# Kernel optimization log

Hardware: AMD Instinct MI355X
Metric: run time of the kernel (lower is better)

Reference implementation:

```python
import jax, jax.numpy as jnp
import numpy as np


def _lstm_layer(x_seq, w_ih, w_hh, b_ih, b_hh):
    # x_seq: [T, in], PyTorch gate order i, f, g, o
    H = w_hh.shape[1]
    h0 = jnp.zeros((H,), x_seq.dtype)

    def step(carry, x_t):
        h, c = carry
        gates = x_t @ w_ih.T + h @ w_hh.T + b_ih + b_hh  # [4H]
        i, f, g, o = jnp.split(gates, 4)
        i = jax.nn.sigmoid(i)
        f = jax.nn.sigmoid(f)
        g = jnp.tanh(g)
        o = jax.nn.sigmoid(o)
        c = f * c + i * g
        h = o * jnp.tanh(c)
        return (h, c), h

    _, hs = jax.lax.scan(step, (h0, h0), x_seq)
    return hs  # [T, H]


def setup_inputs() -> dict:
    key = jax.random.key(0)
    ks = jax.random.split(key, 12)
    B, T, n, H = 8, 128, 32, 128
    s = 1.0 / np.sqrt(H)

    def u(k, shape):
        return jax.random.uniform(k, shape, jnp.float32, -s, s)

    return {
        "x": jax.random.normal(ks[0], (B, T, n, n), jnp.float32),
        "w_ih0": u(ks[1], (4 * H, 1)),
        "w_hh0": u(ks[2], (4 * H, H)),
        "b_ih0": u(ks[3], (4 * H,)),
        "b_hh0": u(ks[4], (4 * H,)),
        "w_ih1": u(ks[5], (4 * H, H)),
        "w_hh1": u(ks[6], (4 * H, H)),
        "b_ih1": u(ks[7], (4 * H,)),
        "b_hh1": u(ks[8], (4 * H,)),
        "w_out": u(ks[9], (1, H)),
        "b_out": u(ks[10], (1,)),
    }


def reference(x, w_ih0, w_hh0, b_ih0, b_hh0, w_ih1, w_hh1, b_ih1, b_hh1, w_out, b_out):
    # x: [B, T, n, n]
    def rnn_forward(xi):  # xi: [T, n, n] -> out [T, 1]
        u = jnp.trace(xi, axis1=-2, axis2=-1)[:, None]  # [T, 1]
        h1 = _lstm_layer(u, w_ih0, w_hh0, b_ih0, b_hh0)
        h2 = _lstm_layer(h1, w_ih1, w_hh1, b_ih1, b_hh1)
        return h2 @ w_out.T + b_out  # [T, 1]

    jac = jax.vmap(jax.jacrev(rnn_forward))(x)  # [B, T, 1, T, n, n]
    d = jnp.diagonal(jac, axis1=1, axis2=3)      # [B, 1, n, n, T]
    # mirror torch: [:, 0] then transpose(2,3).transpose(1,2) -> [B, T, n, n]
    return jnp.transpose(d[:, 0], (0, 3, 1, 2))
```

## Files before the change

### kernel.cpp

```cpp
#include <hip/hip_runtime.h>
#include <math.h>

#define H    128
#define TT   128
#define CH   8
#define NCH  (TT / CH)

#define OFF_H1V   0
#define OFF_PARTS 262144
#define OFF_CNT   1441792

typedef __attribute__((ext_vector_type(2))) float f2;

__device__ __forceinline__ float sigf(float x)       { return 1.0f / (1.0f + __expf(-x)); }
__device__ __forceinline__ float tanhf_fast(float x) { return 1.0f - 2.0f / (1.0f + __expf(2.0f * x)); }

__device__ __forceinline__ float quad_sum(float v) {
    int t = __builtin_amdgcn_update_dpp(0, __float_as_int(v), 0xB1, 0xF, 0xF, true);
    v += __int_as_float(t);
    t = __builtin_amdgcn_update_dpp(0, __float_as_int(v), 0x4E, 0xF, 0xF, true);
    v += __int_as_float(t);
    return v;
}

__device__ __forceinline__ void wait_ge(int* ptr, int val) {
    while (__hip_atomic_load(ptr, __ATOMIC_RELAXED, __HIP_MEMORY_SCOPE_AGENT) < val)
        __builtin_amdgcn_s_sleep(1);
    (void)__hip_atomic_load(ptr, __ATOMIC_ACQUIRE, __HIP_MEMORY_SCOPE_AGENT);
}

#define BARRIER_LGKM() do { \
    asm volatile("s_waitcnt lgkmcnt(0)" ::: "memory"); \
    __builtin_amdgcn_s_barrier(); \
    asm volatile("" ::: "memory"); \
} while (0)

#define BARRIER_ALL() do { \
    asm volatile("s_waitcnt vmcnt(0) lgkmcnt(0)" ::: "memory"); \
    __builtin_amdgcn_s_barrier(); \
    asm volatile("" ::: "memory"); \
} while (0)

#define DECLW4(nm, src) \
    float4 _t_##nm = (src); \
    f2 nm##_a = {_t_##nm.x, _t_##nm.y}; \
    f2 nm##_b = {_t_##nm.z, _t_##nm.w}; \
    asm volatile("" : "+v"(nm##_a), "+v"(nm##_b));

#define LOADW_ALL(W) \
    const float4* wpa_ = (const float4*)((W) + (size_t)(rg)       * H + p * 32); \
    const float4* wpb_ = (const float4*)((W) + (size_t)(rg + 128) * H + p * 32); \
    const float4* wpc_ = (const float4*)((W) + (size_t)(rg + 256) * H + p * 32); \
    const float4* wpd_ = (const float4*)((W) + (size_t)(rg + 384) * H + p * 32); \
    DECLW4(wa0, wpa_[0]) DECLW4(wa1, wpa_[1]) DECLW4(wa2, wpa_[2]) DECLW4(wa3, wpa_[3]) \
    DECLW4(wa4, wpa_[4]) DECLW4(wa5, wpa_[5]) DECLW4(wa6, wpa_[6]) DECLW4(wa7, wpa_[7]) \
    DECLW4(wb0, wpb_[0]) DECLW4(wb1, wpb_[1]) DECLW4(wb2, wpb_[2]) DECLW4(wb3, wpb_[3]) \
    DECLW4(wb4, wpb_[4]) DECLW4(wb5, wpb_[5]) DECLW4(wb6, wpb_[6]) DECLW4(wb7, wpb_[7]) \
    DECLW4(wc0, wpc_[0]) DECLW4(wc1, wpc_[1]) DECLW4(wc2, wpc_[2]) DECLW4(wc3, wpc_[3]) \
    DECLW4(wc4, wpc_[4]) DECLW4(wc5, wpc_[5]) DECLW4(wc6, wpc_[6]) DECLW4(wc7, wpc_[7]) \
    DECLW4(wd0, wpd_[0]) DECLW4(wd1, wpd_[1]) DECLW4(wd2, wpd_[2]) DECLW4(wd3, wpd_[3]) \
    DECLW4(wd4, wpd_[4]) DECLW4(wd5, wpd_[5]) DECLW4(wd6, wpd_[6]) DECLW4(wd7, wpd_[7])

#define PKFMA(acc, w, h) \
    asm("v_pk_fma_f32 %0, %1, %2, %0" : "+v"(acc) : "v"(w), "v"(h));

#define FMA1(nm, hA, hB, acc) PKFMA(acc, nm##_a, hA) PKFMA(acc, nm##_b, hB)

#define DOTJ(j) { \
    f2 hA_ = {hv##j.x, hv##j.y}; f2 hB_ = {hv##j.z, hv##j.w}; \
    FMA1(wa##j, hA_, hB_, q0) FMA1(wb##j, hA_, hB_, q1) \
    FMA1(wc##j, hA_, hB_, q2) FMA1(wd##j, hA_, hB_, q3) }

#define DOT_BODY(HBASE) \
    const float4* _hp4 = (const float4*)(HBASE); \
    float4 hv0=_hp4[0],hv1=_hp4[1],hv2=_hp4[2],hv3=_hp4[3], \
           hv4=_hp4[4],hv5=_hp4[5],hv6=_hp4[6],hv7=_hp4[7]; \
    f2 q0={0.f,0.f},q1={0.f,0.f},q2={0.f,0.f},q3={0.f,0.f}; \
    DOTJ(0) DOTJ(1) DOTJ(2) DOTJ(3) DOTJ(4) DOTJ(5) DOTJ(6) DOTJ(7) \
    float a0=q0.x+q0.y, a1=q1.x+q1.y, a2=q2.x+q2.y, a3=q3.x+q3.y; \
    a0 = quad_sum(a0); a1 = quad_sum(a1); a2 = quad_sum(a2); a3 = quad_sum(a3);

__global__ __launch_bounds__(512)
__attribute__((amdgpu_waves_per_eu(1, 2)))
void pipe_kernel(const float* __restrict__ x,
                 const float* __restrict__ w_ih0,
                 const float* __restrict__ w_hh0,
                 const float* __restrict__ b_ih0,
                 const float* __restrict__ b_hh0,
                 const float* __restrict__ w_ih1,
                 const float* __restrict__ w_hh1,
                 const float* __restrict__ b_ih1,
                 const float* __restrict__ b_hh1,
                 const float* __restrict__ w_out,
                 float* __restrict__ ws,
                 float* __restrict__ outp) {
    const int role = blockIdx.x >> 3;
    const int b    = blockIdx.x & 7;
    const int r    = threadIdx.x;
    const int rg   = r >> 2, p = r & 3;
    const int wsl  = rg >> 5, wpos = rg & 31;

    int* cntA  = (int*)ws + OFF_CNT       + b * 32;
    int* cntB1 = (int*)ws + OFF_CNT + 256 + b * 32;
    int* cntB2 = (int*)ws + OFF_CNT + 512 + b * 32;
    float* h1v = ws + OFF_H1V + (size_t)b * TT * 256;

    __shared__ float hbuf[2][144];
    __shared__ float u_s[TT];
    __shared__ float scr[512];
    __shared__ float hb[CH * 144];
    __shared__ float gbuf[CH][128];

    if (role == 0) {
        LOADW_ALL(w_hh0)
        const float b0 = b_ih0[rg]       + b_hh0[rg];
        const float b1 = b_ih0[rg + 128] + b_hh0[rg + 128];
        const float b2 = b_ih0[rg + 256] + b_hh0[rg + 256];
        const float b3 = b_ih0[rg + 384] + b_hh0[rg + 384];
        const float wi0 = w_ih0[rg], wi1 = w_ih0[rg + 128];
        const float wi2 = w_ih0[rg + 256], wi3 = w_ih0[rg + 384];
        {
            const float* xb = x + (size_t)(b * TT + (r & 127)) * 1024;
            const int pq = r >> 7;
            float u = 0.f;
#pragma unroll
            for (int i = 0; i < 8; i++) u += xb[(pq * 8 + i) * 33];
            scr[r] = u;
        }
        if (r < 144) hbuf[0][r] = 0.f;
        __syncthreads();
        if (r < TT) u_s[r] = scr[r] + scr[r + 128] + scr[r + 256] + scr[r + 384];
        __syncthreads();

        float c1 = 0.f;
        float hn_prev = 0.f, vn_prev = 0.f;
        for (int t = 0; t < TT; t++) {
            if (t > 0) {
                if (p == 0) h1v[(t - 1) * 256 + rg] = hn_prev;
                if (p == 1) h1v[(t - 1) * 256 + 128 + rg] = vn_prev;
            }
            const float u = u_s[t];
            const float* hc = hbuf[t & 1];
            float* hx = hbuf[(t & 1) ^ 1];
            DOT_BODY(hc + p * 36)
            float z0 = a0 + fmaf(wi0, u, b0);
            float z1 = a1 + fmaf(wi1, u, b1);
            float z2 = a2 + fmaf(wi2, u, b2);
            float z3 = a3 + fmaf(wi3, u, b3);
            float gi = sigf(z0), gf = sigf(z1), gg = tanhf_fast(z2), go = sigf(z3);
            float di = gi * (1.f - gi) * wi0, df = gf * (1.f - gf) * wi1;
            float dg = (1.f - gg * gg) * wi2, dd = go * (1.f - go) * wi3;
            float dc = df * c1 + di * gg + gi * dg;
            c1 = gf * c1 + gi * gg;
            float th = tanhf_fast(c1);
            float hn = go * th;
            float vn = dd * th + go * (1.f - th * th) * dc;
            if (p == wsl) hx[p * 36 + wpos] = hn;
            hn_prev = hn; vn_prev = vn;
            if ((t & (CH - 1)) == 0 && t > 0) {
                BARRIER_ALL();
                if (r == 0)
                    __hip_atomic_store(cntA, t, __ATOMIC_RELEASE, __HIP_MEMORY_SCOPE_AGENT);
            } else {
                BARRIER_LGKM();
            }
        }
        if (p == 0) h1v[(TT - 1) * 256 + rg] = hn_prev;
        if (p == 1) h1v[(TT - 1) * 256 + 128 + rg] = vn_prev;
        BARRIER_ALL();
        if (r == 0)
            __hip_atomic_store(cntA, TT, __ATOMIC_RELEASE, __HIP_MEMORY_SCOPE_AGENT);
    } else if (role == 1 || role == 2) {
        LOADW_ALL(w_ih1)
        int* myCnt = (role == 2) ? cntB2 : cntB1;
        const float* hsrc = h1v + ((role == 2) ? 128 : 0);
        float* pbase = ws + OFF_PARTS + (size_t)b * TT * 1024 + ((role == 2) ? 512 : 0);
        for (int c = 0; c < NCH; c++) {
            if (r == 0) wait_ge(cntA, (c + 1) * CH);
            __syncthreads();
            if (r < 256) {
                int tl = r >> 5, k4 = r & 31, s = k4 >> 3, j = k4 & 7;
                float4 v = *(const float4*)(hsrc + (size_t)(c * CH + tl) * 256 + k4 * 4);
                *(float4*)&hb[(tl * 4 + s) * 36 + j * 4] = v;
            }
            __syncthreads();
#pragma unroll
            for (int tl = 0; tl < CH; tl++) {
                DOT_BODY(hb + (tl * 4 + p) * 36)
                float sel = (p == 0) ? a0 : (p == 1) ? a1 : (p == 2) ? a2 : a3;
                pbase[(size_t)(c * CH + tl) * 1024 + r] = sel;
            }
            BARRIER_ALL();
            if (r == 0)
                __hip_atomic_store(myCnt, (c + 1) * CH, __ATOMIC_RELEASE, __HIP_MEMORY_SCOPE_AGENT);
        }
    } else {
        LOADW_ALL(w_hh1)
        const float b0 = b_ih1[rg]       + b_hh1[rg];
        const float b1 = b_ih1[rg + 128] + b_hh1[rg + 128];
        const float b2 = b_ih1[rg + 256] + b_hh1[rg + 256];
        const float b3 = b_ih1[rg + 384] + b_hh1[rg + 384];
        const float wo = w_out[rg];
        if (r < 144) hbuf[0][r] = 0.f;
        __syncthreads();
        const float* parts = ws + OFF_PARTS + (size_t)b * TT * 1024;
        float c2 = 0.f;
        for (int c = 0; c < NCH; c++) {
            if (r == 0) { wait_ge(cntB1, (c + 1) * CH); wait_ge(cntB2, (c + 1) * CH); }
            __syncthreads();
            float4 zf[CH], af[CH];
#pragma unroll
            for (int tl = 0; tl < CH; tl++) {
                zf[tl] = *(const float4*)(parts + (size_t)(c * CH + tl) * 1024 + rg * 4);
                af[tl] = *(const float4*)(parts + (size_t)(c * CH + tl) * 1024 + 512 + rg * 4);
            }
#pragma unroll
            for (int tl = 0; tl < CH; tl++) {
                const int t = c * CH + tl;
                const float* hc = hbuf[t & 1];
                float* hx = hbuf[(t & 1) ^ 1];
                DOT_BODY(hc + p * 36)
                float z0 = a0 + b0 + zf[tl].x;
                float z1 = a1 + b1 + zf[tl].y;
                float z2 = a2 + b2 + zf[tl].z;
                float z3 = a3 + b3 + zf[tl].w;
                float gi = sigf(z0), gf = sigf(z1), gg = tanhf_fast(z2), go = sigf(z3);
                float di = gi * (1.f - gi) * af[tl].x, df = gf * (1.f - gf) * af[tl].y;
                float dg = (1.f - gg * gg) * af[tl].z, dd = go * (1.f - go) * af[tl].w;
                float dc = df * c2 + di * gg + gi * dg;
                c2 = gf * c2 + gi * gg;
                float th = tanhf_fast(c2);
                if (p == wsl) hx[p * 36 + wpos] = go * th;
                float dh2 = dd * th + go * (1.f - th * th) * dc;
                if (p == 0) gbuf[tl][rg] = wo * dh2;
                BARRIER_LGKM();
            }
            {
                const int w = r >> 6, l = r & 63;
                float v = gbuf[w][l] + gbuf[w][l + 64];
                v = quad_sum(v);
                v += __shfl_xor(v, 4, 64);
                v += __shfl_xor(v, 8, 64);
                v += __shfl_xor(v, 16, 64);
                v += __shfl_xor(v, 32, 64);
                if (l == 0) scr[w] = v;
                BARRIER_LGKM();
                if (r < 256) {
                    const int tl = r >> 5, d = r & 31;
                    outp[(size_t)(b * TT + c * CH + tl) * 1024 + d * 33] = scr[tl];
                }
            }
        }
    }
}

extern "C" void kernel_launch(void* const* d_in, const int* in_sizes, int n_in,
                              void* d_out, int out_size, void* d_ws, size_t ws_size,
                              hipStream_t stream) {
    const float* x     = (const float*)d_in[0];
    const float* w_ih0 = (const float*)d_in[1];
    const float* w_hh0 = (const float*)d_in[2];
    const float* b_ih0 = (const float*)d_in[3];
    const float* b_hh0 = (const float*)d_in[4];
    const float* w_ih1 = (const float*)d_in[5];
    const float* w_hh1 = (const float*)d_in[6];
    const float* b_ih1 = (const float*)d_in[7];
    const float* b_hh1 = (const float*)d_in[8];
    const float* w_out = (const float*)d_in[9];

    float* ws = (float*)d_ws;

    hipMemsetAsync(d_out, 0, (size_t)out_size, stream);

    pipe_kernel<<<dim3(32), dim3(512), 0, stream>>>(x, w_ih0, w_hh0, b_ih0, b_hh0,
                                                    w_ih1, w_hh1, b_ih1, b_hh1, w_out,
                                                    ws, (float*)d_out);
}
```

Before: 235.3 us.

## Defer layer-2 output reduction into next chunk and use hardware reciprocal

Double-buffers gbuf so the per-chunk output reduction and store run at the start of the next chunk, sharing the barrier with the wait for producer counters. This removes one barrier per chunk. The two counter waits now run in parallel on different threads instead of one after the other, which shortens the serial spin. The sigmoid and tanh helpers also switch from IEEE division to the approximate hardware reciprocal, which cuts per-step latency but lowers precision slightly.

```diff
diff --git a/kernel.cpp b/kernel.cpp
--- a/kernel.cpp
+++ b/kernel.cpp
@@ -12,8 +12,9 @@
 
 typedef __attribute__((ext_vector_type(2))) float f2;
 
-__device__ __forceinline__ float sigf(float x)       { return 1.0f / (1.0f + __expf(-x)); }
-__device__ __forceinline__ float tanhf_fast(float x) { return 1.0f - 2.0f / (1.0f + __expf(2.0f * x)); }
+__device__ __forceinline__ float rcpf(float x) { return __builtin_amdgcn_rcpf(x); }
+__device__ __forceinline__ float sigf(float x)       { return rcpf(1.0f + __expf(-x)); }
+__device__ __forceinline__ float tanhf_fast(float x) { return 1.0f - 2.0f * rcpf(1.0f + __expf(2.0f * x)); }
 
 __device__ __forceinline__ float quad_sum(float v) {
     int t = __builtin_amdgcn_update_dpp(0, __float_as_int(v), 0xB1, 0xF, 0xF, true);
@@ -109,7 +110,7 @@
     __shared__ float u_s[TT];
     __shared__ float scr[512];
     __shared__ float hb[CH * 144];
-    __shared__ float gbuf[CH][128];
+    __shared__ float gbuf[2][CH][128];
 
     if (role == 0) {
         LOADW_ALL(w_hh0)
@@ -206,8 +207,23 @@
         const float* parts = ws + OFF_PARTS + (size_t)b * TT * 1024;
         float c2 = 0.f;
         for (int c = 0; c < NCH; c++) {
-            if (r == 0) { wait_ge(cntB1, (c + 1) * CH); wait_ge(cntB2, (c + 1) * CH); }
+            if (r == 448) wait_ge(cntB1, (c + 1) * CH);
+            if (r == 449) wait_ge(cntB2, (c + 1) * CH);
+            if (c > 0) {
+                const int w = r >> 6, l = r & 63;
+                float v = gbuf[(c - 1) & 1][w][l] + gbuf[(c - 1) & 1][w][l + 64];
+                v = quad_sum(v);
+                v += __shfl_xor(v, 4, 64);
+                v += __shfl_xor(v, 8, 64);
+                v += __shfl_xor(v, 16, 64);
+                v += __shfl_xor(v, 32, 64);
+                if (l == 0) scr[w] = v;
+            }
             __syncthreads();
+            if (c > 0 && r < 256) {
+                const int tl = r >> 5, d = r & 31;
+                outp[(size_t)(b * TT + (c - 1) * CH + tl) * 1024 + d * 33] = scr[tl];
+            }
             float4 zf[CH], af[CH];
 #pragma unroll
             for (int tl = 0; tl < CH; tl++) {
@@ -232,23 +248,23 @@
                 float th = tanhf_fast(c2);
                 if (p == wsl) hx[p * 36 + wpos] = go * th;
                 float dh2 = dd * th + go * (1.f - th * th) * dc;
-                if (p == 0) gbuf[tl][rg] = wo * dh2;
+                if (p == 0) gbuf[c & 1][tl][rg] = wo * dh2;
                 BARRIER_LGKM();
             }
-            {
-                const int w = r >> 6, l = r & 63;
-                float v = gbuf[w][l] + gbuf[w][l + 64];
-                v = quad_sum(v);
-                v += __shfl_xor(v, 4, 64);
-                v += __shfl_xor(v, 8, 64);
-                v += __shfl_xor(v, 16, 64);
-                v += __shfl_xor(v, 32, 64);
-                if (l == 0) scr[w] = v;
-                BARRIER_LGKM();
-                if (r < 256) {
-                    const int tl = r >> 5, d = r & 31;
-                    outp[(size_t)(b * TT + c * CH + tl) * 1024 + d * 33] = scr[tl];
-                }
+        }
+        {
+            const int w = r >> 6, l = r & 63;
+            float v = gbuf[(NCH - 1) & 1][w][l] + gbuf[(NCH - 1) & 1][w][l + 64];
+            v = quad_sum(v);
+            v += __shfl_xor(v, 4, 64);
+            v += __shfl_xor(v, 8, 64);
+            v += __shfl_xor(v, 16, 64);
+            v += __shfl_xor(v, 32, 64);
+            if (l == 0) scr[w] = v;
+            BARRIER_LGKM();
+            if (r < 256) {
+                const int tl = r >> 5, d = r & 31;
+                outp[(size_t)(b * TT + (NCH - 1) * CH + tl) * 1024 + d * 33] = scr[tl];
             }
         }
     }
```

New measurement: 224.8 us. 4.5% less time.

## Shrink pipeline tail chunks and defer output reduction into next round

Applied to the files above, without the earlier changes.

The last chunk of the layer-0 → input-projection → layer-1 pipeline is split into two half-size chunks, so the downstream stages can start earlier and the serial tail latency shrinks. The layer-1 stage now double-buffers its gradient buffer and folds the previous chunk's cross-row reduction and output scatter into the next round's barrier. This removes one dedicated barrier per chunk from the serial recurrence. The counter waits are spread across two threads. Sigmoid and tanh also switch from a full division to the hardware reciprocal, which lowers ALU latency at a small cost in precision.

```diff
diff --git a/kernel.cpp b/kernel.cpp
--- a/kernel.cpp
+++ b/kernel.cpp
@@ -4,7 +4,6 @@
 #define H    128
 #define TT   128
 #define CH   8
-#define NCH  (TT / CH)
 
 #define OFF_H1V   0
 #define OFF_PARTS 262144
@@ -12,8 +11,9 @@
 
 typedef __attribute__((ext_vector_type(2))) float f2;
 
-__device__ __forceinline__ float sigf(float x)       { return 1.0f / (1.0f + __expf(-x)); }
-__device__ __forceinline__ float tanhf_fast(float x) { return 1.0f - 2.0f / (1.0f + __expf(2.0f * x)); }
+__device__ __forceinline__ float rcpf(float x) { return __builtin_amdgcn_rcpf(x); }
+__device__ __forceinline__ float sigf(float x)       { return rcpf(1.0f + __expf(-x)); }
+__device__ __forceinline__ float tanhf_fast(float x) { return 1.0f - 2.0f * rcpf(1.0f + __expf(2.0f * x)); }
 
 __device__ __forceinline__ float quad_sum(float v) {
     int t = __builtin_amdgcn_update_dpp(0, __float_as_int(v), 0xB1, 0xF, 0xF, true);
@@ -79,6 +79,75 @@
     DOTJ(0) DOTJ(1) DOTJ(2) DOTJ(3) DOTJ(4) DOTJ(5) DOTJ(6) DOTJ(7) \
     float a0=q0.x+q0.y, a1=q1.x+q1.y, a2=q2.x+q2.y, a3=q3.x+q3.y; \
     a0 = quad_sum(a0); a1 = quad_sum(a1); a2 = quad_sum(a2); a3 = quad_sum(a3);
+
+#define B_ROUND(cstart, clen) { \
+    if (r == 0) wait_ge(cntA, (cstart) + (clen)); \
+    __syncthreads(); \
+    if (r < (clen) * 32) { \
+        int tl = r >> 5, k4 = r & 31, s = k4 >> 3, j = k4 & 7; \
+        float4 v = *(const float4*)(hsrc + (size_t)((cstart) + tl) * 256 + k4 * 4); \
+        *(float4*)&hb[(tl * 4 + s) * 36 + j * 4] = v; \
+    } \
+    __syncthreads(); \
+    _Pragma("unroll") \
+    for (int tl = 0; tl < (clen); tl++) { \
+        DOT_BODY(hb + (tl * 4 + p) * 36) \
+        float sel = (p == 0) ? a0 : (p == 1) ? a1 : (p == 2) ? a2 : a3; \
+        pbase[(size_t)((cstart) + tl) * 1024 + r] = sel; \
+    } \
+    BARRIER_ALL(); \
+    if (r == 0) \
+        __hip_atomic_store(myCnt, (cstart) + (clen), __ATOMIC_RELEASE, __HIP_MEMORY_SCOPE_AGENT); }
+
+#define C_REDUCE(pbuf, plen) { \
+    const int w_ = r >> 6, l_ = r & 63; \
+    if (w_ < (plen)) { \
+        float v_ = gbuf[pbuf][w_][l_] + gbuf[pbuf][w_][l_ + 64]; \
+        v_ = quad_sum(v_); \
+        v_ += __shfl_xor(v_, 4, 64);  v_ += __shfl_xor(v_, 8, 64); \
+        v_ += __shfl_xor(v_, 16, 64); v_ += __shfl_xor(v_, 32, 64); \
+        if (l_ == 0) scr[w_] = v_; \
+    } }
+
+#define C_SCATTER(pstart, plen) \
+    if (r < (plen) * 32) { \
+        const int tl_ = r >> 5, d_ = r & 31; \
+        outp[(size_t)(b * TT + (pstart) + tl_) * 1024 + d_ * 33] = scr[tl_]; \
+    }
+
+#define C_ROUND(cstart, clen, cbuf, pstart, plen, pbuf, HASPREV) { \
+    if (r == 448) wait_ge(cntB1, (cstart) + (clen)); \
+    if (r == 449) wait_ge(cntB2, (cstart) + (clen)); \
+    if (HASPREV) { C_REDUCE(pbuf, plen) } \
+    __syncthreads(); \
+    if (HASPREV) { C_SCATTER(pstart, plen) } \
+    float4 zf[CH], af[CH]; \
+    _Pragma("unroll") \
+    for (int tl = 0; tl < (clen); tl++) { \
+        zf[tl] = *(const float4*)(parts + (size_t)((cstart) + tl) * 1024 + rg * 4); \
+        af[tl] = *(const float4*)(parts + (size_t)((cstart) + tl) * 1024 + 512 + rg * 4); \
+    } \
+    _Pragma("unroll") \
+    for (int tl = 0; tl < (clen); tl++) { \
+        const int t = (cstart) + tl; \
+        const float* hc = hbuf[t & 1]; \
+        float* hx = hbuf[(t & 1) ^ 1]; \
+        DOT_BODY(hc + p * 36) \
+        float z0 = a0 + b0 + zf[tl].x; \
+        float z1 = a1 + b1 + zf[tl].y; \
+        float z2 = a2 + b2 + zf[tl].z; \
+        float z3 = a3 + b3 + zf[tl].w; \
+        float gi = sigf(z0), gf = sigf(z1), gg = tanhf_fast(z2), go = sigf(z3); \
+        float di = gi * (1.f - gi) * af[tl].x, df = gf * (1.f - gf) * af[tl].y; \
+        float dg = (1.f - gg * gg) * af[tl].z, dd = go * (1.f - go) * af[tl].w; \
+        float dc = df * c2 + di * gg + gi * dg; \
+        c2 = gf * c2 + gi * gg; \
+        float th = tanhf_fast(c2); \
+        if (p == wsl) hx[p * 36 + wpos] = go * th; \
+        float dh2 = dd * th + go * (1.f - th * th) * dc; \
+        if (p == 0) gbuf[cbuf][tl][rg] = wo * dh2; \
+        BARRIER_LGKM(); \
+    } }
 
 __global__ __launch_bounds__(512)
 __attribute__((amdgpu_waves_per_eu(1, 2)))
@@ -109,7 +178,7 @@
     __shared__ float u_s[TT];
     __shared__ float scr[512];
     __shared__ float hb[CH * 144];
-    __shared__ float gbuf[CH][128];
+    __shared__ float gbuf[2][CH][128];
 
     if (role == 0) {
         LOADW_ALL(w_hh0)
@@ -157,7 +226,7 @@
             float vn = dd * th + go * (1.f - th * th) * dc;
             if (p == wsl) hx[p * 36 + wpos] = hn;
             hn_prev = hn; vn_prev = vn;
-            if ((t & (CH - 1)) == 0 && t > 0) {
+            if (t > 0 && ((t & (CH - 1)) == 0 || t == 124)) {
                 BARRIER_ALL();
                 if (r == 0)
                     __hip_atomic_store(cntA, t, __ATOMIC_RELEASE, __HIP_MEMORY_SCOPE_AGENT);
@@ -175,25 +244,9 @@
         int* myCnt = (role == 2) ? cntB2 : cntB1;
         const float* hsrc = h1v + ((role == 2) ? 128 : 0);
         float* pbase = ws + OFF_PARTS + (size_t)b * TT * 1024 + ((role == 2) ? 512 : 0);
-        for (int c = 0; c < NCH; c++) {
-            if (r == 0) wait_ge(cntA, (c + 1) * CH);
-            __syncthreads();
-            if (r < 256) {
-                int tl = r >> 5, k4 = r & 31, s = k4 >> 3, j = k4 & 7;
-                float4 v = *(const float4*)(hsrc + (size_t)(c * CH + tl) * 256 + k4 * 4);
-                *(float4*)&hb[(tl * 4 + s) * 36 + j * 4] = v;
-            }
-            __syncthreads();
-#pragma unroll
-            for (int tl = 0; tl < CH; tl++) {
-                DOT_BODY(hb + (tl * 4 + p) * 36)
-                float sel = (p == 0) ? a0 : (p == 1) ? a1 : (p == 2) ? a2 : a3;
-                pbase[(size_t)(c * CH + tl) * 1024 + r] = sel;
-            }
-            BARRIER_ALL();
-            if (r == 0)
-                __hip_atomic_store(myCnt, (c + 1) * CH, __ATOMIC_RELEASE, __HIP_MEMORY_SCOPE_AGENT);
-        }
+        for (int c = 0; c < 15; c++) { B_ROUND(c * CH, CH) }
+        B_ROUND(120, 4)
+        B_ROUND(124, 4)
     } else {
         LOADW_ALL(w_hh1)
         const float b0 = b_ih1[rg]       + b_hh1[rg];
@@ -205,51 +258,16 @@
         __syncthreads();
         const float* parts = ws + OFF_PARTS + (size_t)b * TT * 1024;
         float c2 = 0.f;
-        for (int c = 0; c < NCH; c++) {
-            if (r == 0) { wait_ge(cntB1, (c + 1) * CH); wait_ge(cntB2, (c + 1) * CH); }
-            __syncthreads();
-            float4 zf[CH], af[CH];
-#pragma unroll
-            for (int tl = 0; tl < CH; tl++) {
-                zf[tl] = *(const float4*)(parts + (size_t)(c * CH + tl) * 1024 + rg * 4);
-                af[tl] = *(const float4*)(parts + (size_t)(c * CH + tl) * 1024 + 512 + rg * 4);
-            }
-#pragma unroll
-            for (int tl = 0; tl < CH; tl++) {
-                const int t = c * CH + tl;
-                const float* hc = hbuf[t & 1];
-                float* hx = hbuf[(t & 1) ^ 1];
-                DOT_BODY(hc + p * 36)
-                float z0 = a0 + b0 + zf[tl].x;
-                float z1 = a1 + b1 + zf[tl].y;
-                float z2 = a2 + b2 + zf[tl].z;
-                float z3 = a3 + b3 + zf[tl].w;
-                float gi = sigf(z0), gf = sigf(z1), gg = tanhf_fast(z2), go = sigf(z3);
-                float di = gi * (1.f - gi) * af[tl].x, df = gf * (1.f - gf) * af[tl].y;
-                float dg = (1.f - gg * gg) * af[tl].z, dd = go * (1.f - go) * af[tl].w;
-                float dc = df * c2 + di * gg + gi * dg;
-                c2 = gf * c2 + gi * gg;
-                float th = tanhf_fast(c2);
-                if (p == wsl) hx[p * 36 + wpos] = go * th;
-                float dh2 = dd * th + go * (1.f - th * th) * dc;
-                if (p == 0) gbuf[tl][rg] = wo * dh2;
-                BARRIER_LGKM();
-            }
-            {
-                const int w = r >> 6, l = r & 63;
-                float v = gbuf[w][l] + gbuf[w][l + 64];
-                v = quad_sum(v);
-                v += __shfl_xor(v, 4, 64);
-                v += __shfl_xor(v, 8, 64);
-                v += __shfl_xor(v, 16, 64);
-                v += __shfl_xor(v, 32, 64);
-                if (l == 0) scr[w] = v;
-                BARRIER_LGKM();
-                if (r < 256) {
-                    const int tl = r >> 5, d = r & 31;
-                    outp[(size_t)(b * TT + c * CH + tl) * 1024 + d * 33] = scr[tl];
-                }
-            }
+        C_ROUND(0, CH, 0, 0, 0, 0, 0)
+        for (int c = 1; c < 15; c++) {
+            C_ROUND(c * CH, CH, c & 1, (c - 1) * CH, CH, (c - 1) & 1, 1)
+        }
+        C_ROUND(120, 4, 1, 112, CH, 0, 1)
+        C_ROUND(124, 4, 0, 120, 4, 1, 1)
+        {
+            C_REDUCE(0, 4)
+            BARRIER_LGKM();
+            C_SCATTER(124, 4)
         }
     }
 }
```

Result: faster. 218.9 us, median of 2 (-7.0%).
